# Kernel optimization log

Measured on AMD Instinct MI355X. Metric: run time of the kernel, lower is better.

## Reference

```python
import jax, jax.numpy as jnp
import numpy as np

MUL = 32            # multiplicity of each irrep
N_NODES = 16384
N_EDGES = 262144
AVG_NEIGH = 16.0
N_SPECIES = 4
RADIAL_DIM = 8
INV_SQRT3 = 0.5773502691896258  # normalized CG coeff for 1o x 1o -> 0e (dot)


def setup_inputs() -> dict:
    key = jax.random.key(0)
    ks = jax.random.split(key, 14)
    f32 = jnp.float32
    return {
        "node_features": jax.random.normal(ks[0], (N_NODES, 4 * MUL), dtype=f32),
        "edge_sh": jax.random.normal(ks[1], (N_EDGES, 4), dtype=f32),
        "radial_embedding": jax.random.uniform(ks[2], (N_EDGES, RADIAL_DIM), dtype=f32),
        "W_up_s": jax.random.normal(ks[3], (MUL, MUL), dtype=f32),
        "W_up_v": jax.random.normal(ks[4], (MUL, MUL), dtype=f32),
        "W_r1": jax.random.normal(ks[5], (RADIAL_DIM, RADIAL_DIM), dtype=f32),
        "W_r2": jax.random.normal(ks[6], (RADIAL_DIM, 4 * MUL), dtype=f32),
        "W_dn_s": jax.random.normal(ks[7], (2 * MUL, 2 * MUL), dtype=f32),
        "W_dn_v": jax.random.normal(ks[8], (2 * MUL, MUL), dtype=f32),
        "W_sk_s": jax.random.normal(ks[9], (N_SPECIES, MUL, 2 * MUL), dtype=f32),
        "W_sk_v": jax.random.normal(ks[10], (N_SPECIES, MUL, MUL), dtype=f32),
        "senders": jax.random.randint(ks[11], (N_EDGES,), 0, N_NODES),
        "receivers": jax.random.randint(ks[12], (N_EDGES,), 0, N_NODES),
        "node_species": jax.random.randint(ks[13], (N_NODES,), 0, N_SPECIES),
    }


def reference(node_features, edge_sh, radial_embedding, W_up_s, W_up_v,
              W_r1, W_r2, W_dn_s, W_dn_v, W_sk_s, W_sk_v,
              senders, receivers, node_species):
    n = node_features.shape[0]
    # irreps layout: 32x0e (first MUL cols) + 32x1o (next 3*MUL cols)
    s = node_features[:, :MUL]                      # [N, mul]     0e
    v = node_features[:, MUL:].reshape(n, MUL, 3)   # [N, mul, 3]  1o

    # linear_up: per-irrep channel mixing, 1/sqrt(fan_in) normalization
    s1 = (s @ W_up_s) * (MUL ** -0.5)
    v1 = jnp.einsum('nmi,mk->nki', v, W_up_v) * (MUL ** -0.5)

    # gather sender features per edge
    ss = s1[senders]              # [E, mul]
    vs = v1[senders]              # [E, mul, 3]
    yv = edge_sh[:, 1:4]          # 1o part of edge spherical harmonics (0e part dropped in TP)

    # Clebsch-Gordan tensor product, filtered to output irreps {0e, 1o}:
    #   0e x 1o -> 1o ;  1o x 1o -> 0e (dot, coeff 1/sqrt(3)); cross(1e) & 2e dropped
    m_v_tp = ss[:, :, None] * yv[:, None, :]                 # [E, mul, 3]
    m_s_tp = jnp.einsum('emi,ei->em', vs, yv) * INV_SQRT3    # [E, mul]

    # radial MLP -> one scalar weight per irrep instance of the message
    h = jax.nn.silu((radial_embedding @ W_r1) * (RADIAL_DIM ** -0.5))
    w = (h @ W_r2) * (RADIAL_DIM ** -0.5)                    # [E, 4*mul]
    w_ss, w_vs, w_vt, w_st = jnp.split(w, 4, axis=1)

    # message = concat(self-features, tensor-product paths), radially weighted
    m_s = jnp.concatenate([ss * w_ss, m_s_tp * w_st], axis=1)                          # [E, 2*mul]
    m_v = jnp.concatenate([vs * w_vs[:, :, None], m_v_tp * w_vt[:, :, None]], axis=1)  # [E, 2*mul, 3]

    # scatter-add into receiver nodes, divide by sqrt(avg_num_neighbours)
    inv = AVG_NEIGH ** -0.5
    S = jax.ops.segment_sum(m_s, receivers, num_segments=n) * inv                     # [N, 2*mul]
    V = jax.ops.segment_sum(m_v.reshape(m_v.shape[0], -1), receivers,
                            num_segments=n).reshape(n, 2 * MUL, 3) * inv              # [N, 2*mul, 3]

    # linear_down to gate irreps: MUL 0e features + MUL gate scalars, MUL 1o vectors
    g_s = (S @ W_dn_s) * ((2 * MUL) ** -0.5)                                          # [N, 2*mul]
    g_v = jnp.einsum('nmi,mk->nki', V, W_dn_v) * ((2 * MUL) ** -0.5)                  # [N, mul, 3]

    # species-indexed skip connection from the original node features
    sk_s = jnp.einsum('nm,nmk->nk', s, W_sk_s[node_species]) * (MUL ** -0.5)
    sk_v = jnp.einsum('nmi,nmk->nki', v, W_sk_v[node_species]) * (MUL ** -0.5)
    g_s = 0.5 * (g_s + sk_s)
    g_v = 0.5 * (g_v + sk_v)

    # gate nonlinearity: silu on even scalars, silu(gates) multiplies each 1o vector
    feat_s = jax.nn.silu(g_s[:, :MUL])
    gates = jax.nn.silu(g_s[:, MUL:])
    out_v = g_v * gates[:, :, None]
    return jnp.concatenate([feat_s, out_v.reshape(n, 3 * MUL)], axis=1)  # [N, 4*mul]
```

## Files before the change

kernel.cpp:

```cpp
#include <hip/hip_runtime.h>
#include <hip/hip_bf16.h>
#include <hip/hip_fp16.h>

#define N_NODES 16384
#define N_EDGES 262144
#define MUL 32

__device__ __forceinline__ float silu_f(float x) {
    return x / (1.0f + __expf(-x));
}
__device__ __forceinline__ __half2 i2h2(int v) { return __builtin_bit_cast(__half2, v); }
__device__ __forceinline__ int h22i(__half2 v) { return __builtin_bit_cast(int, v); }

__global__ void k_up(const float* __restrict__ nf,
                     const float* __restrict__ Wus,
                     const float* __restrict__ Wuv,
                     __half* __restrict__ up_h,
                     const int* __restrict__ recv,
                     int* __restrict__ counts,
                     int* __restrict__ rank) {
    __shared__ float sh[2][128];
    int node0 = blockIdx.x * 2;
    int t = threadIdx.x;
    if (t < 32) {
        int e = blockIdx.x * 32 + t;
        rank[e] = atomicAdd(&counts[recv[e]], 1);
    }
    sh[t >> 7][t & 127] = nf[(size_t)node0 * 128 + t];
    __syncthreads();
    int local = t >> 7;
    int c = t & 127;
    int m = c >> 2, comp = c & 3;
    const float* row = sh[local];
    float acc = 0.f;
    if (comp == 0) {
        #pragma unroll
        for (int k = 0; k < 32; ++k) acc += row[k] * Wus[k * 32 + m];
    } else {
        int i = comp - 1;
        #pragma unroll
        for (int k = 0; k < 32; ++k) acc += row[32 + k * 3 + i] * Wuv[k * 32 + m];
    }
    up_h[(size_t)(node0 + local) * 128 + c] = __float2half(acc * 0.17677669529663687f);
}

__global__ void k_scan(const int* __restrict__ counts,
                       int* __restrict__ starts) {
    __shared__ int wtot[16];
    __shared__ int woff[16];
    int t = threadIdx.x;
    int lane = t & 63, wid = t >> 6;
    const int4* cp = (const int4*)(counts + t * 16);
    int4 c0 = cp[0], c1 = cp[1], c2 = cp[2], c3 = cp[3];
    int cs[16] = {c0.x,c0.y,c0.z,c0.w,c1.x,c1.y,c1.z,c1.w,
                  c2.x,c2.y,c2.z,c2.w,c3.x,c3.y,c3.z,c3.w};
    int mysum = 0;
    #pragma unroll
    for (int i = 0; i < 16; ++i) mysum += cs[i];
    int incl = mysum;
    #pragma unroll
    for (int off = 1; off < 64; off <<= 1) {
        int y = __shfl_up(incl, off, 64);
        if (lane >= off) incl += y;
    }
    if (lane == 63) wtot[wid] = incl;
    __syncthreads();
    if (t == 0) {
        int run = 0;
        #pragma unroll
        for (int w = 0; w < 16; ++w) { woff[w] = run; run += wtot[w]; }
    }
    __syncthreads();
    int run = woff[wid] + (incl - mysum);
    #pragma unroll
    for (int i = 0; i < 16; ++i) {
        starts[t * 16 + i] = run;
        run += cs[i];
    }
    if (t == 1023) starts[N_NODES] = run;
}

__global__ void k_edges(const float* __restrict__ rad,
                        const float* __restrict__ Wr1,
                        const int* __restrict__ recv,
                        const int* __restrict__ senders,
                        const float* __restrict__ esh,
                        const int* __restrict__ starts,
                        const int* __restrict__ rank,
                        int4* __restrict__ records) {
    int e = blockIdx.x * blockDim.x + threadIdx.x;
    const float4* rp = (const float4*)(rad + (size_t)e * 8);
    float4 a = rp[0], b = rp[1];
    float r[8] = {a.x, a.y, a.z, a.w, b.x, b.y, b.z, b.w};
    float h[8];
    #pragma unroll
    for (int j = 0; j < 8; ++j) {
        float acc = 0.f;
        #pragma unroll
        for (int k = 0; k < 8; ++k) acc += r[k] * Wr1[k * 8 + j];
        h[j] = silu_f(acc * 0.35355339059327373f);
    }
    float4 ey = *(const float4*)(esh + (size_t)e * 4);
    int snd = senders[e];
    int rc = recv[e];
    int pos = starts[rc] + rank[e];
    int4 meta;
    meta.x = snd;
    meta.y = h22i(__floats2half2_rn(ey.y, ey.z));
    meta.z = h22i(__floats2half2_rn(ey.w, 0.f));
    meta.w = 0;
    int4 hp;
    hp.x = h22i(__floats2half2_rn(h[0], h[1]));
    hp.y = h22i(__floats2half2_rn(h[2], h[3]));
    hp.z = h22i(__floats2half2_rn(h[4], h[5]));
    hp.w = h22i(__floats2half2_rn(h[6], h[7]));
    records[2 * (size_t)pos] = meta;
    records[2 * (size_t)pos + 1] = hp;
}

struct Acc {
    float S0, S1, Vv0, Vv1, Vv2, Vt0, Vt1, Vt2;
};
__device__ __forceinline__ void edge_accum(int4 meta, int4 hp, int2 q,
                                           const float* __restrict__ wr2a,
                                           const float* __restrict__ wr2b,
                                           const float* __restrict__ wr2c,
                                           const float* __restrict__ wr2d,
                                           Acc& A) {
    float2 h01 = __half22float2(i2h2(hp.x));
    float2 h23 = __half22float2(i2h2(hp.y));
    float2 h45 = __half22float2(i2h2(hp.z));
    float2 h67 = __half22float2(i2h2(hp.w));
    float h[8] = {h01.x, h01.y, h23.x, h23.y, h45.x, h45.y, h67.x, h67.y};
    float wss = 0.f, wvs = 0.f, wvt = 0.f, wst = 0.f;
    #pragma unroll
    for (int j = 0; j < 8; ++j) {
        wss += h[j] * wr2a[j];
        wvs += h[j] * wr2b[j];
        wvt += h[j] * wr2c[j];
        wst += h[j] * wr2d[j];
    }
    float2 y01 = __half22float2(i2h2(meta.y));
    float2 y2p = __half22float2(i2h2(meta.z));
    float y0 = y01.x, y1 = y01.y, y2 = y2p.x;
    float2 sv0 = __half22float2(i2h2(q.x));
    float2 v12 = __half22float2(i2h2(q.y));
    float ss = sv0.x, v0 = sv0.y, v1v = v12.x, v2 = v12.y;
    float dot = v0 * y0 + v1v * y1 + v2 * y2;
    A.S0 += ss * wss;
    A.S1 += dot * wst;
    A.Vv0 += v0 * wvs; A.Vv1 += v1v * wvs; A.Vv2 += v2 * wvs;
    float tv = ss * wvt;
    A.Vt0 += tv * y0; A.Vt1 += tv * y1; A.Vt2 += tv * y2;
}

__launch_bounds__(256, 4)
__global__ void k_gather(const __half* __restrict__ up_h,
                         const float* __restrict__ nf,
                         const int4* __restrict__ records,
                         const float* __restrict__ Wr2,
                         const int* __restrict__ starts,
                         const float* __restrict__ Wdns,
                         const float* __restrict__ Wdnv,
                         const float* __restrict__ Wsks,
                         const float* __restrict__ Wskv,
                         const int* __restrict__ species,
                         float* __restrict__ out) {
    __shared__ float agg[4][256];
    __shared__ float snode[4][32];
    __shared__ float vnode[4][96];

    int tid = threadIdx.x;
    int w = tid >> 6;
    int lane = tid & 63;
    int sub = lane >> 5;
    int m = lane & 31;
    int node = blockIdx.x * 4 + w;

    int s0 = starts[node], s1 = starts[node + 1];

    const int4 zi4 = make_int4(0,0,0,0);
    const int2 zi2 = make_int2(0,0);

    int ta = s0 + sub, tb = s0 + 2 + sub;
    bool vca = ta < s1, vcb = tb < s1;
    int4 c0 = zi4, c1 = zi4, d0 = zi4, d1 = zi4;
    if (vca) { const int4* p = records + 2 * (size_t)ta; c0 = p[0]; c1 = p[1]; }
    if (vcb) { const int4* p = records + 2 * (size_t)tb; d0 = p[0]; d1 = p[1]; }

    {
        const float* src = nf + (size_t)node * 128;
        #pragma unroll
        for (int it = 0; it < 2; ++it) {
            int c = lane + it * 64;
            float v = src[c];
            if (c < 32) snode[w][c] = v;
            else        vnode[w][c - 32] = v;
        }
    }

    int2 qa = zi2, qb = zi2;
    if (vca) qa = *(const int2*)(up_h + (size_t)c0.x * 128 + m * 4);
    if (vcb) qb = *(const int2*)(up_h + (size_t)d0.x * 128 + m * 4);

    bool vna = ta + 4 < s1, vnb = tb + 4 < s1;
    int4 n0 = zi4, n1 = zi4, e0 = zi4, e1 = zi4;
    if (vna) { const int4* p = records + 2 * (size_t)(ta + 4); n0 = p[0]; n1 = p[1]; }
    if (vnb) { const int4* p = records + 2 * (size_t)(tb + 4); e0 = p[0]; e1 = p[1]; }

    const float s8 = 0.35355339059327373f;
    const float s8s3 = 0.35355339059327373f * 0.5773502691896258f;
    float wr2a[8], wr2b[8], wr2c[8], wr2d[8];
    #pragma unroll
    for (int j = 0; j < 8; ++j) {
        wr2a[j] = Wr2[j * 128 + m] * s8;
        wr2b[j] = Wr2[j * 128 + 32 + m] * s8;
        wr2c[j] = Wr2[j * 128 + 64 + m] * s8;
        wr2d[j] = Wr2[j * 128 + 96 + m] * s8s3;
    }

    Acc A = {0.f,0.f,0.f,0.f,0.f,0.f,0.f,0.f};
    Acc B = {0.f,0.f,0.f,0.f,0.f,0.f,0.f,0.f};

    for (int t0 = s0; t0 < s1; t0 += 4) {
        int2 qna = zi2, qnb = zi2;
        if (vna) qna = *(const int2*)(up_h + (size_t)n0.x * 128 + m * 4);
        if (vnb) qnb = *(const int2*)(up_h + (size_t)e0.x * 128 + m * 4);

        int t2a = t0 + 8 + sub, t2b = t0 + 10 + sub;
        bool v2a = t2a < s1, v2b = t2b < s1;
        int4 p0 = zi4, p1 = zi4, r0 = zi4, r1 = zi4;
        if (v2a) { const int4* p = records + 2 * (size_t)t2a; p0 = p[0]; p1 = p[1]; }
        if (v2b) { const int4* p = records + 2 * (size_t)t2b; r0 = p[0]; r1 = p[1]; }

        if (vca) edge_accum(c0, c1, qa, wr2a, wr2b, wr2c, wr2d, A);
        if (vcb) edge_accum(d0, d1, qb, wr2a, wr2b, wr2c, wr2d, B);

        c0 = n0; c1 = n1; d0 = e0; d1 = e1;
        qa = qna; qb = qnb;
        n0 = p0; n1 = p1; e0 = r0; e1 = r1;
        vca = vna; vcb = vnb; vna = v2a; vnb = v2b;
    }

    float accS0 = A.S0 + B.S0, accS1 = A.S1 + B.S1;
    float accVv0 = A.Vv0 + B.Vv0, accVv1 = A.Vv1 + B.Vv1, accVv2 = A.Vv2 + B.Vv2;
    float accVt0 = A.Vt0 + B.Vt0, accVt1 = A.Vt1 + B.Vt1, accVt2 = A.Vt2 + B.Vt2;

    accS0 += __shfl_xor(accS0, 32, 64);
    accS1 += __shfl_xor(accS1, 32, 64);
    accVv0 += __shfl_xor(accVv0, 32, 64);
    accVv1 += __shfl_xor(accVv1, 32, 64);
    accVv2 += __shfl_xor(accVv2, 32, 64);
    accVt0 += __shfl_xor(accVt0, 32, 64);
    accVt1 += __shfl_xor(accVt1, 32, 64);
    accVt2 += __shfl_xor(accVt2, 32, 64);

    const float inv_neigh = 0.25f;
    if (sub == 0) {
        agg[w][m]               = accS0 * inv_neigh;
        agg[w][32 + m]          = accS1 * inv_neigh;
        agg[w][64 + 3 * m + 0]  = accVv0 * inv_neigh;
        agg[w][64 + 3 * m + 1]  = accVv1 * inv_neigh;
        agg[w][64 + 3 * m + 2]  = accVv2 * inv_neigh;
        agg[w][160 + 3 * m + 0] = accVt0 * inv_neigh;
        agg[w][160 + 3 * m + 1] = accVt1 * inv_neigh;
        agg[w][160 + 3 * m + 2] = accVt2 * inv_neigh;
    }

    const float* S = agg[w];
    const float* V = agg[w] + 64;
    int sp = species[node];

    float gsa = 0.f, gsb = 0.f, gv0 = 0.f, gv1 = 0.f, gv2 = 0.f;
    {
        int mm0 = sub * 32;
        #pragma unroll 4
        for (int k = 0; k < 32; ++k) {
            int mm = mm0 + k;
            float Sm = S[mm];
            gsa += Sm * Wdns[mm * 64 + m];
            gsb += Sm * Wdns[mm * 64 + 32 + m];
            float wv = Wdnv[mm * 32 + m];
            gv0 += V[mm * 3 + 0] * wv;
            gv1 += V[mm * 3 + 1] * wv;
            gv2 += V[mm * 3 + 2] * wv;
        }
    }
    float ska = 0.f, skb = 0.f, skv0 = 0.f, skv1 = 0.f, skv2 = 0.f;
    {
        const float* Ws = Wsks + (size_t)sp * 2048;
        const float* Wv = Wskv + (size_t)sp * 1024;
        int mm0 = sub * 16;
        #pragma unroll 4
        for (int k = 0; k < 16; ++k) {
            int mm = mm0 + k;
            float sm = snode[w][mm];
            ska += sm * Ws[mm * 64 + m];
            skb += sm * Ws[mm * 64 + 32 + m];
            float wv = Wv[mm * 32 + m];
            skv0 += vnode[w][mm * 3 + 0] * wv;
            skv1 += vnode[w][mm * 3 + 1] * wv;
            skv2 += vnode[w][mm * 3 + 2] * wv;
        }
    }
    gsa += __shfl_xor(gsa, 32, 64);
    gsb += __shfl_xor(gsb, 32, 64);
    gv0 += __shfl_xor(gv0, 32, 64);
    gv1 += __shfl_xor(gv1, 32, 64);
    gv2 += __shfl_xor(gv2, 32, 64);
    ska += __shfl_xor(ska, 32, 64);
    skb += __shfl_xor(skb, 32, 64);
    skv0 += __shfl_xor(skv0, 32, 64);
    skv1 += __shfl_xor(skv1, 32, 64);
    skv2 += __shfl_xor(skv2, 32, 64);

    if (sub == 0) {
        const float inv8 = 0.125f;
        const float isq32 = 0.17677669529663687f;
        float a  = 0.5f * (gsa * inv8 + ska * isq32);
        float b  = 0.5f * (gsb * inv8 + skb * isq32);
        float o0 = 0.5f * (gv0 * inv8 + skv0 * isq32);
        float o1 = 0.5f * (gv1 * inv8 + skv1 * isq32);
        float o2 = 0.5f * (gv2 * inv8 + skv2 * isq32);

        float feat = silu_f(a);
        float gate = silu_f(b);
        float* o = out + (size_t)node * 128;
        o[m] = feat;
        o[32 + 3 * m + 0] = o0 * gate;
        o[32 + 3 * m + 1] = o1 * gate;
        o[32 + 3 * m + 2] = o2 * gate;
    }
}

extern "C" void kernel_launch(void* const* d_in, const int* in_sizes, int n_in,
                              void* d_out, int out_size, void* d_ws, size_t ws_size,
                              hipStream_t stream) {
    const float* nf   = (const float*)d_in[0];
    const float* esh  = (const float*)d_in[1];
    const float* rad  = (const float*)d_in[2];
    const float* Wus  = (const float*)d_in[3];
    const float* Wuv  = (const float*)d_in[4];
    const float* Wr1  = (const float*)d_in[5];
    const float* Wr2  = (const float*)d_in[6];
    const float* Wdns = (const float*)d_in[7];
    const float* Wdnv = (const float*)d_in[8];
    const float* Wsks = (const float*)d_in[9];
    const float* Wskv = (const float*)d_in[10];
    const int* senders   = (const int*)d_in[11];
    const int* receivers = (const int*)d_in[12];
    const int* species   = (const int*)d_in[13];
    float* out = (float*)d_out;

    char* ws = (char*)d_ws;
    __half* up_h   = (__half*)(ws);
    int4* records  = (int4*)(ws + (4u << 20));
    int* counts    = (int*)(ws + (12u << 20));
    int* starts    = (int*)(ws + (12u << 20) + 65536);
    int* rank      = (int*)(ws + (13u << 20));

    hipMemsetAsync(counts, 0, 65536, stream);
    k_up<<<N_NODES / 2, 256, 0, stream>>>(nf, Wus, Wuv, up_h, receivers, counts, rank);
    k_scan<<<1, 1024, 0, stream>>>(counts, starts);
    k_edges<<<N_EDGES / 256, 256, 0, stream>>>(rad, Wr1, receivers, senders, esh,
                                               starts, rank, records);
    k_gather<<<N_NODES / 4, 256, 0, stream>>>(up_h, nf, records, Wr2, starts,
                                              Wdns, Wdnv, Wsks, Wskv, species, out);
}
```

Measured before the change: 177.8 us.

## Pad per-node edge segments to multiples of four with zero records

The scan now rounds each node's edge count up to a multiple of four, and k_edges writes zeroed padding records into the gaps plus a 16-record tail. This lets the gather loop drop all per-edge validity predicates and load records and sender features unconditionally, with the loop unrolled by two. Zero records must contribute nothing to the sums (radial weights come out zero) and point at node 0 as a harmless sender. The cost is extra padding traffic and work per node, and the workspace layout is shifted to fit the larger record buffer.

New measurement: 230.8 us. +29.8%, slower.

```diff
diff --git a/kernel.cpp b/kernel.cpp
--- a/kernel.cpp
+++ b/kernel.cpp
@@ -5,6 +5,7 @@
 #define N_NODES 16384
 #define N_EDGES 262144
 #define MUL 32
+#define REC_CAP (N_EDGES + 3 * N_NODES + 16)
 
 __device__ __forceinline__ float silu_f(float x) {
     return x / (1.0f + __expf(-x));
@@ -56,7 +57,10 @@
                   c2.x,c2.y,c2.z,c2.w,c3.x,c3.y,c3.z,c3.w};
     int mysum = 0;
     #pragma unroll
-    for (int i = 0; i < 16; ++i) mysum += cs[i];
+    for (int i = 0; i < 16; ++i) {
+        cs[i] = (cs[i] + 3) & ~3;
+        mysum += cs[i];
+    }
     int incl = mysum;
     #pragma unroll
     for (int off = 1; off < 64; off <<= 1) {
@@ -86,9 +90,26 @@
                         const int* __restrict__ senders,
                         const float* __restrict__ esh,
                         const int* __restrict__ starts,
+                        const int* __restrict__ counts,
                         const int* __restrict__ rank,
                         int4* __restrict__ records) {
     int e = blockIdx.x * blockDim.x + threadIdx.x;
+    const int4 z = make_int4(0, 0, 0, 0);
+
+    if (e < N_NODES) {
+        int st = starts[e] + counts[e];
+        int en = starts[e + 1];
+        for (int p = st; p < en; ++p) {
+            records[2 * (size_t)p] = z;
+            records[2 * (size_t)p + 1] = z;
+        }
+    }
+    if (e < 16) {
+        int total = starts[N_NODES];
+        records[2 * (size_t)(total + e)] = z;
+        records[2 * (size_t)(total + e) + 1] = z;
+    }
+
     const float4* rp = (const float4*)(rad + (size_t)e * 8);
     float4 a = rp[0], b = rp[1];
     float r[8] = {a.x, a.y, a.z, a.w, b.x, b.y, b.z, b.w};
@@ -179,14 +200,10 @@
 
     int s0 = starts[node], s1 = starts[node + 1];
 
-    const int4 zi4 = make_int4(0,0,0,0);
-    const int2 zi2 = make_int2(0,0);
-
-    int ta = s0 + sub, tb = s0 + 2 + sub;
-    bool vca = ta < s1, vcb = tb < s1;
-    int4 c0 = zi4, c1 = zi4, d0 = zi4, d1 = zi4;
-    if (vca) { const int4* p = records + 2 * (size_t)ta; c0 = p[0]; c1 = p[1]; }
-    if (vcb) { const int4* p = records + 2 * (size_t)tb; d0 = p[0]; d1 = p[1]; }
+    int ta = s0 + sub;
+    const int4* rp;
+    rp = records + 2 * (size_t)ta;        int4 c0 = rp[0], c1 = rp[1];
+    rp = records + 2 * (size_t)(ta + 2);  int4 d0 = rp[0], d1 = rp[1];
 
     {
         const float* src = nf + (size_t)node * 128;
@@ -199,14 +216,11 @@
         }
     }
 
-    int2 qa = zi2, qb = zi2;
-    if (vca) qa = *(const int2*)(up_h + (size_t)c0.x * 128 + m * 4);
-    if (vcb) qb = *(const int2*)(up_h + (size_t)d0.x * 128 + m * 4);
-
-    bool vna = ta + 4 < s1, vnb = tb + 4 < s1;
-    int4 n0 = zi4, n1 = zi4, e0 = zi4, e1 = zi4;
-    if (vna) { const int4* p = records + 2 * (size_t)(ta + 4); n0 = p[0]; n1 = p[1]; }
-    if (vnb) { const int4* p = records + 2 * (size_t)(tb + 4); e0 = p[0]; e1 = p[1]; }
+    int2 qa = *(const int2*)(up_h + (size_t)c0.x * 128 + m * 4);
+    int2 qb = *(const int2*)(up_h + (size_t)d0.x * 128 + m * 4);
+
+    rp = records + 2 * (size_t)(ta + 4);  int4 n0 = rp[0], n1 = rp[1];
+    rp = records + 2 * (size_t)(ta + 6);  int4 e0 = rp[0], e1 = rp[1];
 
     const float s8 = 0.35355339059327373f;
     const float s8s3 = 0.35355339059327373f * 0.5773502691896258f;
@@ -222,24 +236,21 @@
     Acc A = {0.f,0.f,0.f,0.f,0.f,0.f,0.f,0.f};
     Acc B = {0.f,0.f,0.f,0.f,0.f,0.f,0.f,0.f};
 
+    #pragma unroll 2
     for (int t0 = s0; t0 < s1; t0 += 4) {
-        int2 qna = zi2, qnb = zi2;
-        if (vna) qna = *(const int2*)(up_h + (size_t)n0.x * 128 + m * 4);
-        if (vnb) qnb = *(const int2*)(up_h + (size_t)e0.x * 128 + m * 4);
-
-        int t2a = t0 + 8 + sub, t2b = t0 + 10 + sub;
-        bool v2a = t2a < s1, v2b = t2b < s1;
-        int4 p0 = zi4, p1 = zi4, r0 = zi4, r1 = zi4;
-        if (v2a) { const int4* p = records + 2 * (size_t)t2a; p0 = p[0]; p1 = p[1]; }
-        if (v2b) { const int4* p = records + 2 * (size_t)t2b; r0 = p[0]; r1 = p[1]; }
-
-        if (vca) edge_accum(c0, c1, qa, wr2a, wr2b, wr2c, wr2d, A);
-        if (vcb) edge_accum(d0, d1, qb, wr2a, wr2b, wr2c, wr2d, B);
+        int2 qna = *(const int2*)(up_h + (size_t)n0.x * 128 + m * 4);
+        int2 qnb = *(const int2*)(up_h + (size_t)e0.x * 128 + m * 4);
+
+        int t2 = t0 + 8 + sub;
+        rp = records + 2 * (size_t)t2;        int4 p0 = rp[0], p1 = rp[1];
+        rp = records + 2 * (size_t)(t2 + 2);  int4 r0 = rp[0], r1 = rp[1];
+
+        edge_accum(c0, c1, qa, wr2a, wr2b, wr2c, wr2d, A);
+        edge_accum(d0, d1, qb, wr2a, wr2b, wr2c, wr2d, B);
 
         c0 = n0; c1 = n1; d0 = e0; d1 = e1;
         qa = qna; qb = qnb;
         n0 = p0; n1 = p1; e0 = r0; e1 = r1;
-        vca = vna; vcb = vnb; vna = v2a; vnb = v2b;
     }
 
     float accS0 = A.S0 + B.S0, accS1 = A.S1 + B.S1;
@@ -355,15 +366,15 @@
     char* ws = (char*)d_ws;
     __half* up_h   = (__half*)(ws);
     int4* records  = (int4*)(ws + (4u << 20));
-    int* counts    = (int*)(ws + (12u << 20));
-    int* starts    = (int*)(ws + (12u << 20) + 65536);
-    int* rank      = (int*)(ws + (13u << 20));
+    int* counts    = (int*)(ws + (14u << 20));
+    int* starts    = (int*)(ws + (14u << 20) + 65536);
+    int* rank      = (int*)(ws + (15u << 20));
 
     hipMemsetAsync(counts, 0, 65536, stream);
     k_up<<<N_NODES / 2, 256, 0, stream>>>(nf, Wus, Wuv, up_h, receivers, counts, rank);
     k_scan<<<1, 1024, 0, stream>>>(counts, starts);
     k_edges<<<N_EDGES / 256, 256, 0, stream>>>(rad, Wr1, receivers, senders, esh,
-                                               starts, rank, records);
+                                               starts, counts, rank, records);
     k_gather<<<N_NODES / 4, 256, 0, stream>>>(up_h, nf, records, Wr2, starts,
                                               Wdns, Wdnv, Wsks, Wskv, species, out);
 }
```
